# Kernel optimization log

Hardware: AMD Instinct MI355X
Metric: run time of the kernel (lower is better)

## Reference

```python
import jax, jax.numpy as jnp
import numpy as np

D_MODEL = 1024
NUM_HEADS = 16
D_K = D_MODEL // NUM_HEADS
B, S = 2, 2048


def setup_inputs() -> dict:
    key = jax.random.key(0)
    ks = jax.random.split(key, 10)
    scale = 1.0 / np.sqrt(D_MODEL)
    inp = {
        "x": jax.random.normal(ks[0], (B, S, D_MODEL), dtype=jnp.float32),
        "mask": jax.random.randint(ks[1], (B, S, S), 0, 2, dtype=jnp.int32),
        "Wq": jax.random.normal(ks[2], (D_MODEL, D_MODEL), dtype=jnp.float32) * scale,
        "bq": jnp.zeros((D_MODEL,), dtype=jnp.float32),
        "Wk": jax.random.normal(ks[3], (D_MODEL, D_MODEL), dtype=jnp.float32) * scale,
        "bk": jnp.zeros((D_MODEL,), dtype=jnp.float32),
        "Wv": jax.random.normal(ks[4], (D_MODEL, D_MODEL), dtype=jnp.float32) * scale,
        "bv": jnp.zeros((D_MODEL,), dtype=jnp.float32),
        "Wo": jax.random.normal(ks[5], (D_MODEL, D_MODEL), dtype=jnp.float32) * scale,
        "bo": jnp.zeros((D_MODEL,), dtype=jnp.float32),
    }
    return inp


def reference(x, mask, Wq, bq, Wk, bk, Wv, bv, Wo, bo):
    # x: [B,S,D]; Linear is x @ W.T + b (torch convention: W is [out,in])
    b, s, _ = x.shape
    def proj(W, bias):
        h = jnp.einsum('bsd,ed->bse', x, W) + bias          # [B,S,D]
        return h.reshape(b, s, NUM_HEADS, D_K).transpose(0, 2, 1, 3)  # [B,H,S,Dk]
    Q = proj(Wq, bq)
    K = proj(Wk, bk)
    V = proj(Wv, bv)
    scores = jnp.einsum('bhqd,bhkd->bhqk', Q, K) / np.sqrt(D_K)  # [B,H,S,S]
    # mask==0 positions get -1e9 (mask broadcast over heads)
    scores = jnp.where(mask[:, None, :, :] == 0, jnp.float32(-1e9), scores)
    attn = jax.nn.softmax(scores, axis=-1)
    # dropout is identity in eval/deterministic mode
    out = jnp.einsum('bhqk,bhkd->bhqd', attn, V)  # [B,H,S,Dk]
    out = out.transpose(0, 2, 1, 3).reshape(b, s, D_MODEL)
    return jnp.einsum('bsd,ed->bse', out, Wo) + bo
```

## Files before the change

### kernel.cpp

```cpp
#include <hip/hip_runtime.h>


#define B_DIM 2
#define S_DIM 2048
#define H_DIM 16
#define DK 64
#define DM 1024
#define MROWS (B_DIM * S_DIM)

#define K_SCALE 0.1803368801111137f

typedef __attribute__((ext_vector_type(8))) short bf16x8;
typedef __attribute__((ext_vector_type(4))) float f32x4;
typedef __attribute__((ext_vector_type(16))) float f32x16;

__device__ __forceinline__ unsigned short f2bf(float f) {
  union { float f; unsigned u; } v; v.f = f;
  unsigned r = v.u + 0x7fffu + ((v.u >> 16) & 1u);
  return (unsigned short)(r >> 16);
}

__device__ __forceinline__ unsigned cvtpk(float lo, float hi_) {
  unsigned r;
  asm("v_cvt_pk_bf16_f32 %0, %1, %2" : "=v"(r) : "v"(lo), "v"(hi_));
  return r;
}

__device__ __forceinline__ float fexp2(float x) {
  float r;
  asm("v_exp_f32 %0, %1" : "=v"(r) : "v"(x));
  return r;
}

__device__ __forceinline__ void async_ld16(unsigned short* lds, const unsigned short* g) {
  __builtin_amdgcn_global_load_lds(
      (const __attribute__((address_space(1))) unsigned int*)g,
      (__attribute__((address_space(3))) unsigned int*)lds,
      16, 0, 0);
}

__device__ __forceinline__ void async_ld4(unsigned* lds, const unsigned* g) {
  __builtin_amdgcn_global_load_lds(
      (const __attribute__((address_space(1))) unsigned int*)g,
      (__attribute__((address_space(3))) unsigned int*)lds,
      4, 0, 0);
}

__global__ __launch_bounds__(256) void conv_kernel(const float* __restrict__ src,
                                                   unsigned short* __restrict__ dst,
                                                   int n4) {
  int i = blockIdx.x * 256 + threadIdx.x;
  if (i < n4) {
    float4 v = ((const float4*)src)[i];
    ushort4 o;
    o.x = f2bf(v.x); o.y = f2bf(v.y); o.z = f2bf(v.z); o.w = f2bf(v.w);
    ((ushort4*)dst)[i] = o;
  }
}

__global__ __launch_bounds__(256) void maskpack_kernel(const int* __restrict__ mask,
                                                       unsigned* __restrict__ mp,
                                                       int nw) {
  int t = blockIdx.x * 256 + threadIdx.x;
  if (t >= nw) return;
  const int4* p = (const int4*)mask + (size_t)t * 8;
  unsigned w = 0;
#pragma unroll
  for (int j = 0; j < 8; ++j) {
    int4 v = p[j];
    w |= (v.x != 0 ? 1u : 0u) << (j * 4 + 0);
    w |= (v.y != 0 ? 1u : 0u) << (j * 4 + 1);
    w |= (v.z != 0 ? 1u : 0u) << (j * 4 + 2);
    w |= (v.w != 0 ? 1u : 0u) << (j * 4 + 3);
  }
  mp[t] = w;
}

template <int MODE>
__global__ __launch_bounds__(256) void gemm_bt_kernel(
    const unsigned short* __restrict__ A, const unsigned short* __restrict__ B,
    const int M, const int N, const int K,
    unsigned short* __restrict__ Qo, unsigned short* __restrict__ Ko,
    unsigned short* __restrict__ Vo,
    const float* __restrict__ bq, const float* __restrict__ bk,
    const float* __restrict__ bv,
    float* __restrict__ fout, const float* __restrict__ fbias) {
  __shared__ unsigned short sA[128 * 32];
  __shared__ unsigned short sB[128 * 32];
  const int t = threadIdx.x;
  const int l = t & 63;
  const int w = t >> 6;
  const int q = l & 15, g = l >> 4;
  const int wr = w >> 1, wc = w & 1;
  const int nbn = N >> 7;
  const int mb = blockIdx.x / nbn;
  const int nb = blockIdx.x % nbn;

  const f32x4 fzero = {0.f, 0.f, 0.f, 0.f};
  f32x4 acc[4][4];
#pragma unroll
  for (int i = 0; i < 4; ++i)
#pragma unroll
    for (int j = 0; j < 4; ++j) acc[i][j] = fzero;

  const int steps = K >> 5;
  for (int kb = 0; kb < steps; ++kb) {
#pragma unroll
    for (int i = 0; i < 2; ++i) {
      const int idx = i * 256 + t;
      const int row = idx >> 2;
      const int c8 = (idx & 3) * 8;
      async_ld16(&sA[idx * 8], A + (mb * 128 + row) * K + kb * 32 + c8);
      async_ld16(&sB[idx * 8], B + (nb * 128 + row) * K + kb * 32 + c8);
    }
    __syncthreads();
    bf16x8 af[4], bfr[4];
#pragma unroll
    for (int mi = 0; mi < 4; ++mi)
      af[mi] = *(const bf16x8*)&sA[(wr * 64 + mi * 16 + q) * 32 + g * 8];
#pragma unroll
    for (int nj = 0; nj < 4; ++nj)
      bfr[nj] = *(const bf16x8*)&sB[(wc * 64 + nj * 16 + q) * 32 + g * 8];
#pragma unroll
    for (int mi = 0; mi < 4; ++mi)
#pragma unroll
      for (int nj = 0; nj < 4; ++nj)
        acc[mi][nj] = __builtin_amdgcn_mfma_f32_16x16x32_bf16(af[mi], bfr[nj],
                                                              acc[mi][nj], 0, 0, 0);
    __syncthreads();
  }

#pragma unroll
  for (int mi = 0; mi < 4; ++mi) {
    const int mbase = mb * 128 + wr * 64 + mi * 16 + g * 4;
#pragma unroll
    for (int nj = 0; nj < 4; ++nj) {
      const int n = nb * 128 + wc * 64 + nj * 16 + q;
      f32x4 c = acc[mi][nj];
      if (MODE == 0) {
        const int which = n >> 10;
        const int e = n & 1023;
        const int h = e >> 6, dk = e & 63;
        const float bias = (which == 0 ? bq : which == 1 ? bk : bv)[e];
        if (which == 2) {
          const int bi = mbase >> 11, s = mbase & 2047;
          const int bh2 = bi * H_DIM + h;
          ushort4 v4;
          v4.x = f2bf(c[0] + bias);
          v4.y = f2bf(c[1] + bias);
          v4.z = f2bf(c[2] + bias);
          v4.w = f2bf(c[3] + bias);
          *(ushort4*)&Vo[((size_t)bh2 * DK + dk) * S_DIM + s] = v4;
        } else {
          unsigned short* dst = (which == 0) ? Qo : Ko;
          const float scl = (which == 0) ? 1.0f : K_SCALE;
#pragma unroll
          for (int r = 0; r < 4; ++r) {
            const int m = mbase + r;
            const int bi = m >> 11, s = m & 2047;
            dst[((size_t)(bi * H_DIM + h) * S_DIM + s) * DK + dk] =
                f2bf((c[r] + bias) * scl);
          }
        }
      } else {
        const float bias = fbias[n];
#pragma unroll
        for (int r = 0; r < 4; ++r) {
          const int m = mbase + r;
          fout[(size_t)m * N + n] = c[r] + bias;
        }
      }
    }
  }
}

__global__ __launch_bounds__(256) void attn_kernel(
    const unsigned short* __restrict__ Qb, const unsigned short* __restrict__ Kb,
    const unsigned short* __restrict__ Vtb, const unsigned* __restrict__ mp,
    unsigned short* __restrict__ Ob) {
  __shared__ unsigned short sK[2][2048];
  __shared__ unsigned short sV[2][2048];
  __shared__ unsigned smask[2][128];

  const int t = threadIdx.x, l = t & 63, w = t >> 6;
  const int bh = blockIdx.x >> 4;
  const int qb = blockIdx.x & 15;
  const int qbase = qb * 128 + w * 32;
  const int b = bh >> 4, h = bh & 15;
  const int q = l & 31, hi = l >> 5;

  const unsigned short* Qh = Qb + (size_t)bh * S_DIM * DK;
  const unsigned short* Kh = Kb + (size_t)bh * S_DIM * DK;
  const unsigned short* Vh = Vtb + (size_t)bh * DK * S_DIM;

  const int rS = t >> 3;
  const int cgS = (t & 7) ^ (rS & 7);
  const unsigned short* gK = Kh + rS * DK + cgS * 8;
  const int dV = rS + 32 * (cgS >> 2);
  const unsigned short* gV = Vh + (size_t)dV * S_DIM + (cgS & 3) * 8;
  const unsigned* gm = mp + ((size_t)b * S_DIM + qb * 128 + w * 64 + l) * (S_DIM / 32);

  bf16x8 qf[4];
#pragma unroll
  for (int ds = 0; ds < 4; ++ds)
    qf[ds] = *(const bf16x8*)(Qh + (qbase + q) * DK + ds * 16 + hi * 8);

  float l_run = 0.f;
  f32x16 accT0 = {0.f,0.f,0.f,0.f,0.f,0.f,0.f,0.f,0.f,0.f,0.f,0.f,0.f,0.f,0.f,0.f};
  f32x16 accT1 = accT0;
  const f32x16 zero16 = accT0;
  const int swz = q & 7;

  async_ld16(&sK[0][t * 8], gK);
  async_ld16(&sV[0][t * 8], gV);
  if (w < 2) async_ld4(&smask[0][w * 64 + l], gm);
  __syncthreads();

  for (int kt = 0; kt < 64; ++kt) {
    const int cur = kt & 1;
    if (kt < 63) {
      const int ktn = kt + 1;
      async_ld16(&sK[cur ^ 1][t * 8], gK + ktn * 2048);
      async_ld16(&sV[cur ^ 1][t * 8], gV + ktn * 32);
      if (w < 2) async_ld4(&smask[cur ^ 1][w * 64 + l], gm + ktn);
    }

    bf16x8 ck[4];
#pragma unroll
    for (int ds = 0; ds < 4; ++ds)
      ck[ds] = *(const bf16x8*)&sK[cur][q * 64 + (((ds * 2 + hi) ^ swz) * 8)];
    bf16x8 cv[2][2];
#pragma unroll
    for (int dt = 0; dt < 2; ++dt)
#pragma unroll
      for (int st = 0; st < 2; ++st)
        cv[dt][st] = *(const bf16x8*)&sV[cur][q * 64 + (((dt * 4 + st * 2 + hi) ^ swz) * 8)];
    const unsigned cmw = smask[cur][w * 32 + q];

    f32x16 T = zero16;
    T = __builtin_amdgcn_mfma_f32_32x32x16_bf16(ck[0], qf[0], T, 0, 0, 0);
    T = __builtin_amdgcn_mfma_f32_32x32x16_bf16(ck[1], qf[1], T, 0, 0, 0);
    T = __builtin_amdgcn_mfma_f32_32x32x16_bf16(ck[2], qf[2], T, 0, 0, 0);
    T = __builtin_amdgcn_mfma_f32_32x32x16_bf16(ck[3], qf[3], T, 0, 0, 0);

    const unsigned mws = cmw >> (4 * hi);
    float p[16];
    float ts = 0.f;
#pragma unroll
    for (int r = 0; r < 16; ++r) {
      const int c = (r & 3) + 8 * (r >> 2);
      const float e = fexp2(T[r]);
      p[r] = ((mws >> c) & 1u) ? e : 0.f;
      ts += p[r];
    }
    ts += __shfl_xor(ts, 32, 64);
    l_run += ts;

    unsigned pw[8];
#pragma unroll
    for (int st = 0; st < 2; ++st) {
      const int r0 = st * 8;
      unsigned a0 = cvtpk(p[r0 + 0], p[r0 + 1]);
      unsigned a1 = cvtpk(p[r0 + 2], p[r0 + 3]);
      unsigned a2 = cvtpk(p[r0 + 4], p[r0 + 5]);
      unsigned a3 = cvtpk(p[r0 + 6], p[r0 + 7]);
      asm("v_permlane32_swap_b32 %0, %1" : "+v"(a0), "+v"(a2));
      asm("v_permlane32_swap_b32 %0, %1" : "+v"(a1), "+v"(a3));
      pw[st * 4 + 0] = a0;
      pw[st * 4 + 1] = a1;
      pw[st * 4 + 2] = a2;
      pw[st * 4 + 3] = a3;
    }
    union { unsigned u[4]; bf16x8 v; } pf0, pf1;
    pf0.u[0] = pw[0]; pf0.u[1] = pw[1]; pf0.u[2] = pw[2]; pf0.u[3] = pw[3];
    pf1.u[0] = pw[4]; pf1.u[1] = pw[5]; pf1.u[2] = pw[6]; pf1.u[3] = pw[7];

    accT0 = __builtin_amdgcn_mfma_f32_32x32x16_bf16(cv[0][0], pf0.v, accT0, 0, 0, 0);
    accT0 = __builtin_amdgcn_mfma_f32_32x32x16_bf16(cv[0][1], pf1.v, accT0, 0, 0, 0);
    accT1 = __builtin_amdgcn_mfma_f32_32x32x16_bf16(cv[1][0], pf0.v, accT1, 0, 0, 0);
    accT1 = __builtin_amdgcn_mfma_f32_32x32x16_bf16(cv[1][1], pf1.v, accT1, 0, 0, 0);

    __syncthreads();
  }

  const float linv = 1.0f / l_run;
  unsigned short* orow = Ob + ((size_t)b * S_DIM + qbase + q) * DM + h * DK;
#pragma unroll
  for (int dt = 0; dt < 2; ++dt) {
#pragma unroll
    for (int rp = 0; rp < 8; ++rp) {
      const int r = rp * 2;
      const int d0 = (r & 3) + 8 * (r >> 2) + 4 * hi;
      const float v0 = (dt ? accT1[r] : accT0[r]) * linv;
      const float v1 = (dt ? accT1[r + 1] : accT0[r + 1]) * linv;
      *(unsigned*)&orow[dt * 32 + d0] = cvtpk(v0, v1);
    }
  }
}

extern "C" void kernel_launch(void* const* d_in, const int* in_sizes, int n_in,
                              void* d_out, int out_size, void* d_ws, size_t ws_size,
                              hipStream_t stream) {
  (void)in_sizes; (void)n_in; (void)out_size; (void)ws_size;
  const float* x  = (const float*)d_in[0];
  const int* mask = (const int*)d_in[1];
  const float* Wq = (const float*)d_in[2];
  const float* bq = (const float*)d_in[3];
  const float* Wk = (const float*)d_in[4];
  const float* bk = (const float*)d_in[5];
  const float* Wv = (const float*)d_in[6];
  const float* bv = (const float*)d_in[7];
  const float* Wo = (const float*)d_in[8];
  const float* bo = (const float*)d_in[9];
  float* out = (float*)d_out;

  char* ws = (char*)d_ws;
  unsigned short* Xb   = (unsigned short*)(ws + 0);
  unsigned short* Wqkv = (unsigned short*)(ws + (8u << 20));
  unsigned short* Wob  = (unsigned short*)(ws + 14680064);
  unsigned short* Qbuf = (unsigned short*)(ws + 16777216);
  unsigned short* Kbuf = (unsigned short*)(ws + 25165824);
  unsigned short* Vtb  = (unsigned short*)(ws + 33554432);
  unsigned short* Obuf = (unsigned short*)(ws + 41943040);
  unsigned* Mp         = (unsigned*)(ws + 50331648);

  conv_kernel<<<4096, 256, 0, stream>>>(x, Xb, 1048576);
  conv_kernel<<<1024, 256, 0, stream>>>(Wq, Wqkv + 0 * 1048576, 262144);
  conv_kernel<<<1024, 256, 0, stream>>>(Wk, Wqkv + 1 * 1048576, 262144);
  conv_kernel<<<1024, 256, 0, stream>>>(Wv, Wqkv + 2 * 1048576, 262144);
  conv_kernel<<<1024, 256, 0, stream>>>(Wo, Wob, 262144);
  maskpack_kernel<<<1024, 256, 0, stream>>>(mask, Mp, 262144);
  gemm_bt_kernel<0><<<32 * 24, 256, 0, stream>>>(Xb, Wqkv, MROWS, 3 * DM, DM,
                                                 Qbuf, Kbuf, Vtb, bq, bk, bv,
                                                 nullptr, nullptr);
  attn_kernel<<<512, 256, 0, stream>>>(Qbuf, Kbuf, Vtb, Mp, Obuf);
  gemm_bt_kernel<1><<<32 * 8, 256, 0, stream>>>(Obuf, Wob, MROWS, DM, DM,
                                                nullptr, nullptr, nullptr,
                                                nullptr, nullptr, nullptr,
                                                out, bo);
}
```

Before: 260.2 us.

## Split attention over KV halves with combine kernel; merge prep kernels into one launch

Attention now runs as two independent halves over the key sequence. This doubles the block count from 512 to 1024 so more work is in flight per CU. Each half writes unnormalised bf16 partial outputs and row sums, and a new combine kernel adds them and normalises. The five convert launches and the mask-pack launch are also fused into one prep kernel to cut launch overhead. The trade-off is extra global traffic for the partial buffers, one more launch, and correctness that relies on both halves using a compatible (fixed) softmax offset.

```diff
diff --git a/kernel.cpp b/kernel.cpp
--- a/kernel.cpp
+++ b/kernel.cpp
@@ -20,6 +20,12 @@
   return (unsigned short)(r >> 16);
 }
 
+__device__ __forceinline__ float bf2f(short x) {
+  union { unsigned u; float f; } v;
+  v.u = ((unsigned)(unsigned short)x) << 16;
+  return v.f;
+}
+
 __device__ __forceinline__ unsigned cvtpk(float lo, float hi_) {
   unsigned r;
   asm("v_cvt_pk_bf16_f32 %0, %1, %2" : "=v"(r) : "v"(lo), "v"(hi_));
@@ -46,34 +52,40 @@
       4, 0, 0);
 }
 
-__global__ __launch_bounds__(256) void conv_kernel(const float* __restrict__ src,
-                                                   unsigned short* __restrict__ dst,
-                                                   int n4) {
-  int i = blockIdx.x * 256 + threadIdx.x;
-  if (i < n4) {
+__global__ __launch_bounds__(256) void prep_kernel(
+    const float* __restrict__ x, const float* __restrict__ Wq,
+    const float* __restrict__ Wk, const float* __restrict__ Wv,
+    const float* __restrict__ Wo, const int* __restrict__ mask,
+    unsigned short* __restrict__ Xb, unsigned short* __restrict__ Wqkv,
+    unsigned short* __restrict__ Wob, unsigned* __restrict__ Mp) {
+  const int bid = blockIdx.x, tid = threadIdx.x;
+  if (bid < 8192) {
+    const float* src;
+    unsigned short* dst;
+    int i;
+    if (bid < 4096)      { src = x;  dst = Xb;             i = bid * 256 + tid; }
+    else if (bid < 5120) { src = Wq; dst = Wqkv;           i = (bid - 4096) * 256 + tid; }
+    else if (bid < 6144) { src = Wk; dst = Wqkv + 1048576; i = (bid - 5120) * 256 + tid; }
+    else if (bid < 7168) { src = Wv; dst = Wqkv + 2097152; i = (bid - 6144) * 256 + tid; }
+    else                 { src = Wo; dst = Wob;            i = (bid - 7168) * 256 + tid; }
     float4 v = ((const float4*)src)[i];
     ushort4 o;
     o.x = f2bf(v.x); o.y = f2bf(v.y); o.z = f2bf(v.z); o.w = f2bf(v.w);
     ((ushort4*)dst)[i] = o;
-  }
-}
-
-__global__ __launch_bounds__(256) void maskpack_kernel(const int* __restrict__ mask,
-                                                       unsigned* __restrict__ mp,
-                                                       int nw) {
-  int t = blockIdx.x * 256 + threadIdx.x;
-  if (t >= nw) return;
-  const int4* p = (const int4*)mask + (size_t)t * 8;
-  unsigned w = 0;
-#pragma unroll
-  for (int j = 0; j < 8; ++j) {
-    int4 v = p[j];
-    w |= (v.x != 0 ? 1u : 0u) << (j * 4 + 0);
-    w |= (v.y != 0 ? 1u : 0u) << (j * 4 + 1);
-    w |= (v.z != 0 ? 1u : 0u) << (j * 4 + 2);
-    w |= (v.w != 0 ? 1u : 0u) << (j * 4 + 3);
-  }
-  mp[t] = w;
+  } else {
+    const int t = (bid - 8192) * 256 + tid;
+    const int4* p = (const int4*)mask + (size_t)t * 8;
+    unsigned w = 0;
+#pragma unroll
+    for (int j = 0; j < 8; ++j) {
+      int4 v = p[j];
+      w |= (v.x != 0 ? 1u : 0u) << (j * 4 + 0);
+      w |= (v.y != 0 ? 1u : 0u) << (j * 4 + 1);
+      w |= (v.z != 0 ? 1u : 0u) << (j * 4 + 2);
+      w |= (v.w != 0 ? 1u : 0u) << (j * 4 + 3);
+    }
+    Mp[t] = w;
+  }
 }
 
 template <int MODE>
@@ -174,20 +186,26 @@
   }
 }
 
+template <int SPLIT>
 __global__ __launch_bounds__(256) void attn_kernel(
     const unsigned short* __restrict__ Qb, const unsigned short* __restrict__ Kb,
     const unsigned short* __restrict__ Vtb, const unsigned* __restrict__ mp,
-    unsigned short* __restrict__ Ob) {
+    unsigned short* __restrict__ Ob, unsigned short* __restrict__ Op,
+    float* __restrict__ Lp) {
   __shared__ unsigned short sK[2][2048];
   __shared__ unsigned short sV[2][2048];
   __shared__ unsigned smask[2][128];
 
   const int t = threadIdx.x, l = t & 63, w = t >> 6;
-  const int bh = blockIdx.x >> 4;
-  const int qb = blockIdx.x & 15;
+  int blk = blockIdx.x, sp = 0;
+  if (SPLIT == 2) { sp = blk & 1; blk >>= 1; }
+  const int bh = blk >> 4;
+  const int qb = blk & 15;
   const int qbase = qb * 128 + w * 32;
   const int b = bh >> 4, h = bh & 15;
   const int q = l & 31, hi = l >> 5;
+  const int NT = (SPLIT == 2) ? 32 : 64;
+  const int spT = sp * 32;
 
   const unsigned short* Qh = Qb + (size_t)bh * S_DIM * DK;
   const unsigned short* Kh = Kb + (size_t)bh * S_DIM * DK;
@@ -195,10 +213,10 @@
 
   const int rS = t >> 3;
   const int cgS = (t & 7) ^ (rS & 7);
-  const unsigned short* gK = Kh + rS * DK + cgS * 8;
+  const unsigned short* gK = Kh + rS * DK + cgS * 8 + (size_t)spT * 2048;
   const int dV = rS + 32 * (cgS >> 2);
-  const unsigned short* gV = Vh + (size_t)dV * S_DIM + (cgS & 3) * 8;
-  const unsigned* gm = mp + ((size_t)b * S_DIM + qb * 128 + w * 64 + l) * (S_DIM / 32);
+  const unsigned short* gV = Vh + (size_t)dV * S_DIM + (cgS & 3) * 8 + spT * 32;
+  const unsigned* gm = mp + ((size_t)b * S_DIM + qb * 128 + w * 64 + l) * (S_DIM / 32) + spT;
 
   bf16x8 qf[4];
 #pragma unroll
@@ -216,9 +234,9 @@
   if (w < 2) async_ld4(&smask[0][w * 64 + l], gm);
   __syncthreads();
 
-  for (int kt = 0; kt < 64; ++kt) {
+  for (int kt = 0; kt < NT; ++kt) {
     const int cur = kt & 1;
-    if (kt < 63) {
+    if (kt < NT - 1) {
       const int ktn = kt + 1;
       async_ld16(&sK[cur ^ 1][t * 8], gK + ktn * 2048);
       async_ld16(&sV[cur ^ 1][t * 8], gV + ktn * 32);
@@ -283,25 +301,66 @@
     __syncthreads();
   }
 
-  const float linv = 1.0f / l_run;
-  unsigned short* orow = Ob + ((size_t)b * S_DIM + qbase + q) * DM + h * DK;
-#pragma unroll
-  for (int dt = 0; dt < 2; ++dt) {
-#pragma unroll
-    for (int rp = 0; rp < 8; ++rp) {
-      const int r = rp * 2;
-      const int d0 = (r & 3) + 8 * (r >> 2) + 4 * hi;
-      const float v0 = (dt ? accT1[r] : accT0[r]) * linv;
-      const float v1 = (dt ? accT1[r + 1] : accT0[r + 1]) * linv;
-      *(unsigned*)&orow[dt * 32 + d0] = cvtpk(v0, v1);
-    }
-  }
+  if (SPLIT == 2) {
+    unsigned short* orow = Op + (size_t)sp * 4194304 +
+                           ((size_t)b * S_DIM + qbase + q) * DM + h * DK;
+#pragma unroll
+    for (int dt = 0; dt < 2; ++dt) {
+#pragma unroll
+      for (int rp = 0; rp < 8; ++rp) {
+        const int r = rp * 2;
+        const int d0 = (r & 3) + 8 * (r >> 2) + 4 * hi;
+        const float v0 = (dt ? accT1[r] : accT0[r]);
+        const float v1 = (dt ? accT1[r + 1] : accT0[r + 1]);
+        *(unsigned*)&orow[dt * 32 + d0] = cvtpk(v0, v1);
+      }
+    }
+    if (hi == 0) Lp[sp * 65536 + bh * 2048 + qbase + q] = l_run;
+  } else {
+    const float linv = 1.0f / l_run;
+    unsigned short* orow = Ob + ((size_t)b * S_DIM + qbase + q) * DM + h * DK;
+#pragma unroll
+    for (int dt = 0; dt < 2; ++dt) {
+#pragma unroll
+      for (int rp = 0; rp < 8; ++rp) {
+        const int r = rp * 2;
+        const int d0 = (r & 3) + 8 * (r >> 2) + 4 * hi;
+        const float v0 = (dt ? accT1[r] : accT0[r]) * linv;
+        const float v1 = (dt ? accT1[r + 1] : accT0[r + 1]) * linv;
+        *(unsigned*)&orow[dt * 32 + d0] = cvtpk(v0, v1);
+      }
+    }
+  }
+}
+
+__global__ __launch_bounds__(256) void combine_kernel(
+    const unsigned short* __restrict__ Op, const float* __restrict__ Lp,
+    unsigned short* __restrict__ Ob) {
+  const int tid = blockIdx.x * 256 + threadIdx.x;
+  const int row = tid >> 7;
+  const int c8 = (tid & 127) * 8;
+  const int b = row >> 11, s = row & 2047;
+  const int h = c8 >> 6;
+  const float l0 = Lp[(b * 16 + h) * 2048 + s];
+  const float l1 = Lp[65536 + (b * 16 + h) * 2048 + s];
+  const float inv = 1.0f / (l0 + l1);
+  const size_t base = (size_t)row * DM + c8;
+  const bf16x8 p0 = *(const bf16x8*)&Op[base];
+  const bf16x8 p1 = *(const bf16x8*)&Op[4194304 + base];
+  union { unsigned u[4]; bf16x8 v; } o;
+#pragma unroll
+  for (int i = 0; i < 4; ++i) {
+    const float v0 = (bf2f(p0[2 * i]) + bf2f(p1[2 * i])) * inv;
+    const float v1 = (bf2f(p0[2 * i + 1]) + bf2f(p1[2 * i + 1])) * inv;
+    o.u[i] = cvtpk(v0, v1);
+  }
+  *(bf16x8*)&Ob[base] = o.v;
 }
 
 extern "C" void kernel_launch(void* const* d_in, const int* in_sizes, int n_in,
                               void* d_out, int out_size, void* d_ws, size_t ws_size,
                               hipStream_t stream) {
-  (void)in_sizes; (void)n_in; (void)out_size; (void)ws_size;
+  (void)in_sizes; (void)n_in; (void)out_size;
   const float* x  = (const float*)d_in[0];
   const int* mask = (const int*)d_in[1];
   const float* Wq = (const float*)d_in[2];
@@ -323,17 +382,23 @@
   unsigned short* Vtb  = (unsigned short*)(ws + 33554432);
   unsigned short* Obuf = (unsigned short*)(ws + 41943040);
   unsigned* Mp         = (unsigned*)(ws + 50331648);
-
-  conv_kernel<<<4096, 256, 0, stream>>>(x, Xb, 1048576);
-  conv_kernel<<<1024, 256, 0, stream>>>(Wq, Wqkv + 0 * 1048576, 262144);
-  conv_kernel<<<1024, 256, 0, stream>>>(Wk, Wqkv + 1 * 1048576, 262144);
-  conv_kernel<<<1024, 256, 0, stream>>>(Wv, Wqkv + 2 * 1048576, 262144);
-  conv_kernel<<<1024, 256, 0, stream>>>(Wo, Wob, 262144);
-  maskpack_kernel<<<1024, 256, 0, stream>>>(mask, Mp, 262144);
+  unsigned short* Opart = (unsigned short*)(ws + 51380224);
+  float* Lpart         = (float*)(ws + 68157440);
+  const bool can_split = ws_size >= 68681728;
+
+  prep_kernel<<<9216, 256, 0, stream>>>(x, Wq, Wk, Wv, Wo, mask,
+                                        Xb, Wqkv, Wob, Mp);
   gemm_bt_kernel<0><<<32 * 24, 256, 0, stream>>>(Xb, Wqkv, MROWS, 3 * DM, DM,
                                                  Qbuf, Kbuf, Vtb, bq, bk, bv,
                                                  nullptr, nullptr);
-  attn_kernel<<<512, 256, 0, stream>>>(Qbuf, Kbuf, Vtb, Mp, Obuf);
+  if (can_split) {
+    attn_kernel<2><<<1024, 256, 0, stream>>>(Qbuf, Kbuf, Vtb, Mp,
+                                             nullptr, Opart, Lpart);
+    combine_kernel<<<2048, 256, 0, stream>>>(Opart, Lpart, Obuf);
+  } else {
+    attn_kernel<1><<<512, 256, 0, stream>>>(Qbuf, Kbuf, Vtb, Mp,
+                                            Obuf, nullptr, nullptr);
+  }
   gemm_bt_kernel<1><<<32 * 8, 256, 0, stream>>>(Obuf, Wob, MROWS, DM, DM,
                                                 nullptr, nullptr, nullptr,
                                                 nullptr, nullptr, nullptr,
```

After: 257.3 us. No clear change (-1.1%).
